# Kernel tuning notes

Measured on AMD Instinct MI355X. Metric: run time of the kernel, lower is better.

## Reference

```python
import jax, jax.numpy as jnp
import numpy as np

B, D, T = 32, 6, 2048
FH, ENC, H, CONF, NC, K = 128, 128, 256, 64, 10, 5


def setup_inputs() -> dict:
    key = jax.random.key(0)
    ks = iter(jax.random.split(key, 40))
    n = lambda shape, s=0.05: jax.random.normal(next(ks), shape, dtype=jnp.float32) * s
    inp = {
        'M': jax.random.normal(next(ks), (B, D, T), dtype=jnp.float32),
        # causal conv frontend (4 dilated convs, kernel 5)
        'conv_w0': n((FH, D, K)), 'conv_b0': n((FH,)),
        'conv_w1': n((FH, FH, K)), 'conv_b1': n((FH,)),
        'conv_w2': n((FH, FH, K)), 'conv_b2': n((FH,)),
        'conv_w3': n((FH, FH, K)), 'conv_b3': n((FH,)),
        # encoder projection
        'enc_w': n((ENC, FH)), 'enc_b': n((ENC,)),
        # selective state space
        'A': n((H, H), 0.01), 'ip_w': n((H, ENC)), 'ip_b': n((H,)),
        'state_bias': jnp.zeros((H,), jnp.float32),
        'op_w': n((H, H)), 'op_b': n((H,)),
        # classifier head
        'cls_w1': n((256, H)), 'cls_b1': n((256,)),
        'cls_w2': n((NC, 256)), 'cls_b2': n((NC,)),
        # metanet: 2*D -> 64 -> 128 -> confound_dim
        'mn_w1': n((64, 2 * D)), 'mn_b1': n((64,)),
        'mn_w2': n((128, 64)), 'mn_b2': n((128,)),
        'mn_w3': n((CONF, 128)), 'mn_b3': n((CONF,)),
        # frontdoor: confound_dim -> 128 -> ssm_hidden
        'fd_w1': n((128, CONF)), 'fd_b1': n((128,)),
        'fd_w2': n((H, 128)), 'fd_b2': n((H,)),
    }
    return inp


def _causal_conv(x, w, b, d):
    # x: (B,C,T), w: (O,I,K). pad-left (K-1)*d == pad-both + trim-right in torch code
    y = jax.lax.conv_general_dilated(
        x, w, window_strides=(1,), padding=[((w.shape[2] - 1) * d, 0)],
        rhs_dilation=(d,), dimension_numbers=('NCH', 'OIH', 'NCH'))
    return jax.nn.relu(y + b[None, :, None])


def reference(M, conv_w0, conv_b0, conv_w1, conv_b1, conv_w2, conv_b2, conv_w3, conv_b3,
              enc_w, enc_b, A, ip_w, ip_b, state_bias, op_w, op_b,
              cls_w1, cls_b1, cls_w2, cls_b2,
              mn_w1, mn_b1, mn_w2, mn_b2, mn_w3, mn_b3,
              fd_w1, fd_b1, fd_w2, fd_b2):
    # frontend: 4 causal dilated convs with ReLU
    out = M
    for w, b, d in ((conv_w0, conv_b0, 1), (conv_w1, conv_b1, 2),
                    (conv_w2, conv_b2, 4), (conv_w3, conv_b3, 8)):
        out = _causal_conv(out, w, b, d)
    feat = jnp.einsum('bct,ec->bte', out, enc_w) + enc_b  # (B,T,ENC)
    # SSM: precompute input projection, then sequential scan over T
    u = jnp.einsum('bte,he->bth', feat, ip_w) + ip_b + state_bias  # (B,T,H)

    def step(h, ut):
        h = jax.nn.gelu(h @ A.T + ut, approximate=False)
        return h, h

    h0 = jnp.zeros((M.shape[0], A.shape[0]), M.dtype)
    _, hs = jax.lax.scan(step, h0, jnp.swapaxes(u, 0, 1))  # hs: (T,B,H)
    ssm_out = jnp.einsum('tbh,gh->btg', hs, op_w) + op_b  # (B,T,H)
    pooled = ssm_out.mean(axis=1)  # (B,H)
    logits = jax.nn.relu(pooled @ cls_w1.T + cls_b1) @ cls_w2.T + cls_b2
    # confounder summary: mean & unbiased std over time
    s = jnp.concatenate([M.mean(axis=2), jnp.std(M, axis=2, ddof=1)], axis=1)
    z = jax.nn.relu(s @ mn_w1.T + mn_b1)
    z = jax.nn.relu(z @ mn_w2.T + mn_b2)
    conf_hat = z @ mn_w3.T + mn_b3
    adj = jax.nn.relu(conf_hat @ fd_w1.T + fd_b1) @ fd_w2.T + fd_b2
    corrected = pooled - adj
    return (logits, pooled, corrected, conf_hat)
```

## Files before the change

### kernel.cpp

```cpp
#include <hip/hip_runtime.h>
#include <cmath>


typedef __bf16 bf16_t;
typedef bf16_t bf16x8 __attribute__((ext_vector_type(8)));
typedef float f32x4 __attribute__((ext_vector_type(4)));

__device__ __forceinline__ f32x4 mfma16(bf16x8 a, bf16x8 b, f32x4 c) {
  return __builtin_amdgcn_mfma_f32_16x16x32_bf16(a, b, c, 0, 0, 0);
}

__device__ __forceinline__ float gelu_f(float x) {
  float a = x * 0.70710678118654752440f;
  float z = fabsf(a);
  float t = __builtin_amdgcn_rcpf(1.0f + 0.3275911f * z);
  float p = t * (0.254829592f +
            t * (-0.284496736f +
            t * (1.421413741f +
            t * (-1.453152027f +
            t * 1.061405429f))));
  float e = __expf(-z * z);
  float erf_a = __builtin_copysignf(1.0f - p * e, a);
  return 0.5f * x * (1.0f + erf_a);
}

__global__ void k_prep(const float* __restrict__ w0, const float* __restrict__ w1,
                       const float* __restrict__ w2, const float* __restrict__ w3,
                       const float* __restrict__ ip_w, const float* __restrict__ enc_w,
                       const float* __restrict__ enc_b, const float* __restrict__ ip_b,
                       const float* __restrict__ sbias,
                       bf16_t* __restrict__ wb0, bf16_t* __restrict__ wb1,
                       bf16_t* __restrict__ wb2, bf16_t* __restrict__ wb3,
                       bf16_t* __restrict__ wce, float* __restrict__ bce) {
  int bid = blockIdx.x;
  if (bid >= 976) {
    int idx = (bid - 976) * 256 + threadIdx.x;
    int h = idx >> 7, c = idx & 127;
    float s = 0.f;
    for (int e = 0; e < 128; ++e) s += ip_w[h * 128 + e] * enc_w[e * 128 + c];
    wce[h * 128 + c] = (bf16_t)s;
    if (c == 0) {
      float bv = 0.f;
      for (int e = 0; e < 128; ++e) bv += ip_w[h * 128 + e] * enc_b[e];
      bce[h] = bv + ip_b[h] + sbias[h];
    }
    return;
  }
  int idx = bid * 256 + threadIdx.x;
  if (idx < 128 * 32) {
    int o = idx >> 5, k = idx & 31;
    float v = 0.f;
    if (k < 30) { int i = k / 5, kk = k - i * 5; v = w0[(o * 6 + i) * 5 + kk]; }
    wb0[idx] = (bf16_t)v;
    return;
  }
  int e = idx - 128 * 32;
  if (e < 3 * 5 * 128 * 128) {
    int layer = e / (5 * 128 * 128);
    int r = e - layer * (5 * 128 * 128);
    int ks = r / 16384;
    int o = (r >> 7) & 127;
    int i = r & 127;
    const float* w = layer == 0 ? w1 : layer == 1 ? w2 : w3;
    bf16_t* wb = layer == 0 ? wb1 : layer == 1 ? wb2 : wb3;
    wb[r] = (bf16_t)w[(o * 128 + i) * 5 + ks];
  }
}

__global__ __launch_bounds__(256) void k_conv0(const float* __restrict__ M,
                                               const bf16_t* __restrict__ wb0,
                                               const float* __restrict__ b0,
                                               bf16_t* __restrict__ out) {
  __shared__ float raw[6][136];
  __shared__ bf16_t Xe[128 * 40];
  const int tid = threadIdx.x;
  const int b = blockIdx.y, t0 = blockIdx.x * 128;
  for (int id = tid; id < 6 * 132; id += 256) {
    int i = id / 132, j = id - i * 132;
    int t = t0 - 4 + j;
    raw[i][j] = (t >= 0) ? M[((size_t)b * 6 + i) * 2048 + t] : 0.f;
  }
  __syncthreads();
  for (int id = tid; id < 128 * 32; id += 256) {
    int tl = id >> 5, k = id & 31;
    float v = 0.f;
    if (k < 30) { int i = k / 5, kk = k - i * 5; v = raw[i][tl + kk]; }
    Xe[tl * 40 + k] = (bf16_t)v;
  }
  __syncthreads();
  const int w = tid >> 6, lane = tid & 63, q = lane >> 4, l15 = lane & 15;
  const int k0 = q * 8;
  const f32x4 z4 = {0.f, 0.f, 0.f, 0.f};
  f32x4 acc[2][8];
#pragma unroll
  for (int mt = 0; mt < 2; ++mt)
#pragma unroll
    for (int nt = 0; nt < 8; ++nt) acc[mt][nt] = z4;
  bf16x8 af[2];
#pragma unroll
  for (int mt = 0; mt < 2; ++mt)
    af[mt] = *(const bf16x8*)&Xe[(w * 32 + mt * 16 + l15) * 40 + k0];
#pragma unroll
  for (int nt = 0; nt < 8; ++nt) {
    bf16x8 bf = *(const bf16x8*)&wb0[(nt * 16 + l15) * 32 + k0];
#pragma unroll
    for (int mt = 0; mt < 2; ++mt) acc[mt][nt] = mfma16(af[mt], bf, acc[mt][nt]);
  }
#pragma unroll
  for (int nt = 0; nt < 8; ++nt) {
    const int o = nt * 16 + l15;
    const float bias = b0[o];
#pragma unroll
    for (int mt = 0; mt < 2; ++mt) {
#pragma unroll
      for (int r = 0; r < 4; ++r) {
        int t = t0 + w * 32 + mt * 16 + q * 4 + r;
        float v = acc[mt][nt][r] + bias;
        out[((size_t)b * 2048 + t) * 128 + o] = (bf16_t)(v > 0.f ? v : 0.f);
      }
    }
  }
}

template <int DIL>
__global__ __launch_bounds__(256) void k_conv(const bf16_t* __restrict__ in,
                                              const bf16_t* __restrict__ wb,
                                              const float* __restrict__ bias,
                                              bf16_t* __restrict__ out) {
  __shared__ bf16_t Xs[160 * 136];
  const int tid = threadIdx.x;
  const int b = blockIdx.y, t0 = blockIdx.x * 128;
  const bf16_t* src = in + (size_t)b * 2048 * 128;
  for (int id = tid; id < 160 * 16; id += 256) {
    int r = id >> 4, ck = id & 15;
    int t = t0 + r - 32;
    int4 v = make_int4(0, 0, 0, 0);
    if (t >= 0) v = *(const int4*)(src + (size_t)t * 128 + ck * 8);
    *(int4*)&Xs[r * 136 + ck * 8] = v;
  }
  __syncthreads();
  const int w = tid >> 6, lane = tid & 63, q = lane >> 4, l15 = lane & 15;
  const f32x4 z4 = {0.f, 0.f, 0.f, 0.f};
  f32x4 acc[2][8];
#pragma unroll
  for (int mt = 0; mt < 2; ++mt)
#pragma unroll
    for (int nt = 0; nt < 8; ++nt) acc[mt][nt] = z4;
#pragma unroll
  for (int ks = 0; ks < 5; ++ks) {
    const int shift = (4 - ks) * DIL;
#pragma unroll
    for (int kt = 0; kt < 4; ++kt) {
      const int k0 = kt * 32 + q * 8;
      bf16x8 af[2];
#pragma unroll
      for (int mt = 0; mt < 2; ++mt)
        af[mt] = *(const bf16x8*)&Xs[(32 + w * 32 + mt * 16 + l15 - shift) * 136 + k0];
#pragma unroll
      for (int nt = 0; nt < 8; ++nt) {
        bf16x8 bf = *(const bf16x8*)&wb[((size_t)ks * 128 + nt * 16 + l15) * 128 + k0];
#pragma unroll
        for (int mt = 0; mt < 2; ++mt) acc[mt][nt] = mfma16(af[mt], bf, acc[mt][nt]);
      }
    }
  }
#pragma unroll
  for (int nt = 0; nt < 8; ++nt) {
    const int o = nt * 16 + l15;
    const float bv = bias[o];
#pragma unroll
    for (int mt = 0; mt < 2; ++mt) {
#pragma unroll
      for (int r = 0; r < 4; ++r) {
        int t = t0 + w * 32 + mt * 16 + q * 4 + r;
        float v = acc[mt][nt][r] + bv;
        out[((size_t)b * 2048 + t) * 128 + o] = (bf16_t)(v > 0.f ? v : 0.f);
      }
    }
  }
}

__global__ __launch_bounds__(256) void k_ugemm(const bf16_t* __restrict__ in,
                                               const bf16_t* __restrict__ wce,
                                               const float* __restrict__ bce,
                                               bf16_t* __restrict__ u) {
  __shared__ bf16_t Xs[128 * 136];
  const int tid = threadIdx.x;
  const int b = blockIdx.y, t0 = blockIdx.x * 128, hh = blockIdx.z;
  const bf16_t* src = in + (size_t)b * 2048 * 128;
  for (int id = tid; id < 128 * 16; id += 256) {
    int r = id >> 4, ck = id & 15;
    *(int4*)&Xs[r * 136 + ck * 8] = *(const int4*)(src + (size_t)(t0 + r) * 128 + ck * 8);
  }
  __syncthreads();
  const int w = tid >> 6, lane = tid & 63, q = lane >> 4, l15 = lane & 15;
  const f32x4 z4 = {0.f, 0.f, 0.f, 0.f};
  f32x4 acc[2][8];
#pragma unroll
  for (int mt = 0; mt < 2; ++mt)
#pragma unroll
    for (int nt = 0; nt < 8; ++nt) acc[mt][nt] = z4;
#pragma unroll
  for (int kt = 0; kt < 4; ++kt) {
    const int k0 = kt * 32 + q * 8;
    bf16x8 af[2];
#pragma unroll
    for (int mt = 0; mt < 2; ++mt)
      af[mt] = *(const bf16x8*)&Xs[(w * 32 + mt * 16 + l15) * 136 + k0];
#pragma unroll
    for (int nt = 0; nt < 8; ++nt) {
      bf16x8 bf = *(const bf16x8*)&wce[((size_t)hh * 128 + nt * 16 + l15) * 128 + k0];
#pragma unroll
      for (int mt = 0; mt < 2; ++mt) acc[mt][nt] = mfma16(af[mt], bf, acc[mt][nt]);
    }
  }
#pragma unroll
  for (int nt = 0; nt < 8; ++nt) {
    const int h = hh * 128 + nt * 16 + l15;
    const float bv = bce[h];
#pragma unroll
    for (int mt = 0; mt < 2; ++mt) {
#pragma unroll
      for (int r = 0; r < 4; ++r) {
        int t = t0 + w * 32 + mt * 16 + q * 4 + r;
        u[((size_t)b * 2048 + t) * 256 + h] = (bf16_t)(acc[mt][nt][r] + bv);
      }
    }
  }
}

__global__ __launch_bounds__(256, 1) void k_scan(const float* __restrict__ Am,
                                                 const bf16_t* __restrict__ u,
                                                 float* __restrict__ hbarOut) {
  __shared__ bf16_t hb[2][256];
  const int b = blockIdx.x;
  const int tid = threadIdx.x;
  const int w = tid >> 6, lane = tid & 63, q = lane >> 4, l15 = lane & 15;

  bf16x8 bfr[4][8];
#pragma unroll
  for (int nt = 0; nt < 4; ++nt) {
    const int c = w * 64 + nt * 16 + l15;
#pragma unroll
    for (int kt = 0; kt < 8; ++kt) {
      const float* ap = Am + (size_t)c * 256 + kt * 32 + q * 8;
      f32x4 p0 = *(const f32x4*)ap;
      f32x4 p1 = *(const f32x4*)(ap + 4);
      bf16x8 v;
      v[0] = (bf16_t)p0[0]; v[1] = (bf16_t)p0[1]; v[2] = (bf16_t)p0[2]; v[3] = (bf16_t)p0[3];
      v[4] = (bf16_t)p1[0]; v[5] = (bf16_t)p1[1]; v[6] = (bf16_t)p1[2]; v[7] = (bf16_t)p1[3];
      bfr[nt][kt] = v;
    }
  }
  hb[0][tid] = (bf16_t)0.f;
  hb[1][tid] = (bf16_t)0.f;
  const bf16_t* up = u + (size_t)b * 2048 * 256 + tid;
  float hbar = 0.f;
  bf16_t ua = up[0];
  bf16_t ub = up[256];
  __syncthreads();

  const f32x4 z4 = {0.f, 0.f, 0.f, 0.f};

#define SCAN_STEP(RD, WR, UREG)                                   \
  {                                                               \
    bf16x8 af[8];                                                 \
    _Pragma("unroll")                                             \
    for (int kt = 0; kt < 8; ++kt)                                \
      af[kt] = *(const bf16x8*)&hb[RD][kt * 32 + q * 8];          \
    float uin = (float)(UREG);                                    \
    f32x4 acc[4];                                                 \
    _Pragma("unroll")                                             \
    for (int nt = 0; nt < 4; ++nt) {                              \
      acc[nt] = z4;                                               \
      acc[nt][0] = (q == nt) ? uin : 0.f;                         \
    }                                                             \
    _Pragma("unroll")                                             \
    for (int kt = 0; kt < 8; ++kt) {                              \
      _Pragma("unroll")                                           \
      for (int nt = 0; nt < 4; ++nt)                              \
        acc[nt] = mfma16(af[kt], bfr[nt][kt], acc[nt]);           \
    }                                                             \
    __builtin_amdgcn_sched_group_barrier(0x100, 8, 0);            \
    __builtin_amdgcn_sched_group_barrier(0x008, 32, 0);           \
    float y = (q == 0) ? acc[0][0] : (q == 1) ? acc[1][0]         \
            : (q == 2) ? acc[2][0] : acc[3][0];                   \
    float g = gelu_f(y);                                          \
    hb[WR][tid] = (bf16_t)g;                                      \
    asm volatile("s_waitcnt lgkmcnt(0)" ::: "memory");            \
    __builtin_amdgcn_s_barrier();                                 \
    __builtin_amdgcn_sched_barrier(0);                            \
    hbar += g;                                                    \
  }

  for (int t = 0; t < 2048; t += 2) {
    bf16_t ua2 = (t + 2 < 2048) ? up[(size_t)(t + 2) * 256] : (bf16_t)0.f;
    SCAN_STEP(0, 1, ua)
    bf16_t ub2 = (t + 3 < 2048) ? up[(size_t)(t + 3) * 256] : (bf16_t)0.f;
    SCAN_STEP(1, 0, ub)
    ua = ua2;
    ub = ub2;
  }
#undef SCAN_STEP

  hbarOut[b * 256 + tid] = hbar * (1.f / 2048.f);
}

__global__ __launch_bounds__(256) void k_post(
    const float* __restrict__ M, const float* __restrict__ hbar,
    const float* __restrict__ w1, const float* __restrict__ b1,
    const float* __restrict__ w2, const float* __restrict__ b2,
    const float* __restrict__ w3, const float* __restrict__ b3,
    const float* __restrict__ f1, const float* __restrict__ fb1,
    const float* __restrict__ f2, const float* __restrict__ fb2,
    const float* __restrict__ op_w, const float* __restrict__ op_b,
    const float* __restrict__ cw1, const float* __restrict__ cb1,
    const float* __restrict__ cw2, const float* __restrict__ cb2,
    float* __restrict__ out) {
  const int b = blockIdx.x, tid = threadIdx.x;
  const int w = tid >> 6, lane = tid & 63;
  __shared__ float s12[12], z1[64], z2[128], ch[64], a1[128], adjs[256];
  __shared__ float hs[256], ps[256], hid[256];
  __shared__ float as_[4], ass_[4];
  for (int c = 0; c < 6; ++c) {
    const float* p = M + ((size_t)b * 6 + c) * 2048;
    float s = 0.f, ss = 0.f;
    for (int t = tid; t < 2048; t += 256) { float v = p[t]; s += v; ss += v * v; }
    for (int o = 32; o > 0; o >>= 1) { s += __shfl_down(s, o, 64); ss += __shfl_down(ss, o, 64); }
    if (lane == 0) { as_[w] = s; ass_[w] = ss; }
    __syncthreads();
    if (tid == 0) {
      s = as_[0] + as_[1] + as_[2] + as_[3];
      ss = ass_[0] + ass_[1] + ass_[2] + ass_[3];
      float mean = s * (1.f / 2048.f);
      float var = (ss - 2048.f * mean * mean) * (1.f / 2047.f);
      if (var < 0.f) var = 0.f;
      s12[c] = mean;
      s12[6 + c] = sqrtf(var);
    }
    __syncthreads();
  }
  if (tid < 64) {
    float v = b1[tid];
    for (int e = 0; e < 12; ++e) v += w1[tid * 12 + e] * s12[e];
    z1[tid] = v > 0.f ? v : 0.f;
  }
  __syncthreads();
  if (tid < 128) {
    float v = b2[tid];
    for (int e = 0; e < 64; ++e) v += w2[tid * 64 + e] * z1[e];
    z2[tid] = v > 0.f ? v : 0.f;
  }
  __syncthreads();
  if (tid < 64) {
    float v = b3[tid];
    for (int e = 0; e < 128; ++e) v += w3[tid * 128 + e] * z2[e];
    ch[tid] = v;
    out[16704 + b * 64 + tid] = v;
  }
  __syncthreads();
  if (tid < 128) {
    float v = fb1[tid];
    for (int e = 0; e < 64; ++e) v += f1[tid * 64 + e] * ch[e];
    a1[tid] = v > 0.f ? v : 0.f;
  }
  __syncthreads();
  {
    float v = fb2[tid];
    for (int e = 0; e < 128; ++e) v += f2[tid * 128 + e] * a1[e];
    adjs[tid] = v;
  }
  hs[tid] = hbar[b * 256 + tid];
  __syncthreads();
  float v = op_b[tid];
  for (int h = 0; h < 256; ++h) v += op_w[tid * 256 + h] * hs[h];
  out[320 + b * 256 + tid] = v;
  out[8512 + b * 256 + tid] = v - adjs[tid];
  ps[tid] = v;
  __syncthreads();
  float hv = cb1[tid];
  for (int h = 0; h < 256; ++h) hv += cw1[tid * 256 + h] * ps[h];
  hid[tid] = hv > 0.f ? hv : 0.f;
  __syncthreads();
  if (tid < 10) {
    float lv = cb2[tid];
    for (int h = 0; h < 256; ++h) lv += cw2[tid * 256 + h] * hid[h];
    out[b * 10 + tid] = lv;
  }
}

extern "C" void kernel_launch(void* const* d_in, const int* in_sizes, int n_in,
                              void* d_out, int out_size, void* d_ws, size_t ws_size,
                              hipStream_t stream) {
  (void)in_sizes; (void)n_in; (void)out_size; (void)ws_size;
  const float* M    = (const float*)d_in[0];
  const float* w0   = (const float*)d_in[1];  const float* b0  = (const float*)d_in[2];
  const float* w1   = (const float*)d_in[3];  const float* b1  = (const float*)d_in[4];
  const float* w2   = (const float*)d_in[5];  const float* b2  = (const float*)d_in[6];
  const float* w3   = (const float*)d_in[7];  const float* b3  = (const float*)d_in[8];
  const float* encw = (const float*)d_in[9];  const float* encb = (const float*)d_in[10];
  const float* Am   = (const float*)d_in[11];
  const float* ipw  = (const float*)d_in[12]; const float* ipb = (const float*)d_in[13];
  const float* sb   = (const float*)d_in[14];
  const float* opw  = (const float*)d_in[15]; const float* opb = (const float*)d_in[16];
  const float* cw1  = (const float*)d_in[17]; const float* cb1 = (const float*)d_in[18];
  const float* cw2  = (const float*)d_in[19]; const float* cb2 = (const float*)d_in[20];
  const float* mw1  = (const float*)d_in[21]; const float* mb1 = (const float*)d_in[22];
  const float* mw2  = (const float*)d_in[23]; const float* mb2 = (const float*)d_in[24];
  const float* mw3  = (const float*)d_in[25]; const float* mb3 = (const float*)d_in[26];
  const float* fw1  = (const float*)d_in[27]; const float* fb1 = (const float*)d_in[28];
  const float* fw2  = (const float*)d_in[29]; const float* fb2 = (const float*)d_in[30];
  float* out = (float*)d_out;

  char* ws = (char*)d_ws;
  bf16_t* wb0  = (bf16_t*)(ws + 0);
  bf16_t* wb1  = (bf16_t*)(ws + 8192);
  bf16_t* wb2  = (bf16_t*)(ws + 172032);
  bf16_t* wb3  = (bf16_t*)(ws + 335872);
  bf16_t* wce  = (bf16_t*)(ws + 499712);
  float*  bce  = (float*) (ws + 565248);
  float*  hbar = (float*) (ws + 566272);
  bf16_t* actA = (bf16_t*)(ws + 633856);
  bf16_t* actB = (bf16_t*)(ws + 17411072);
  bf16_t* u    = (bf16_t*)(ws + 34188288);

  k_prep<<<1104, 256, 0, stream>>>(w0, w1, w2, w3, ipw, encw, encb, ipb, sb,
                                   wb0, wb1, wb2, wb3, wce, bce);
  k_conv0<<<dim3(16, 32), 256, 0, stream>>>(M, wb0, b0, actA);
  k_conv<2><<<dim3(16, 32), 256, 0, stream>>>(actA, wb1, b1, actB);
  k_conv<4><<<dim3(16, 32), 256, 0, stream>>>(actB, wb2, b2, actA);
  k_conv<8><<<dim3(16, 32), 256, 0, stream>>>(actA, wb3, b3, actB);
  k_ugemm<<<dim3(16, 32, 2), 256, 0, stream>>>(actB, wce, bce, u);
  k_scan<<<32, 256, 0, stream>>>(Am, u, hbar);
  k_post<<<32, 256, 0, stream>>>(M, hbar, mw1, mb1, mw2, mb2, mw3, mb3,
                                 fw1, fb1, fw2, fb2, opw, opb,
                                 cw1, cb1, cw2, cb2, out);
}
```

Baseline: 1.407 ms.

## Split scan step across 16 waves with one output tile per wave

The sequential SSM scan block grows from 4 to 16 waves. Each wave now owns a single 16-column tile of A and issues 8 MFMAs per step instead of 32, so the per-step dependent chain is shorter and the matrix work is spread over more SIMDs. In exchange the per-step block barrier now synchronises 16 waves instead of 4, and only a quarter of the lanes do useful GELU and stores.

```diff
diff --git a/kernel.cpp b/kernel.cpp
--- a/kernel.cpp
+++ b/kernel.cpp
@@ -229,32 +229,31 @@
   }
 }
 
-__global__ __launch_bounds__(256, 1) void k_scan(const float* __restrict__ Am,
-                                                 const bf16_t* __restrict__ u,
-                                                 float* __restrict__ hbarOut) {
+__global__ __launch_bounds__(1024, 1) void k_scan(const float* __restrict__ Am,
+                                                  const bf16_t* __restrict__ u,
+                                                  float* __restrict__ hbarOut) {
   __shared__ bf16_t hb[2][256];
   const int b = blockIdx.x;
   const int tid = threadIdx.x;
   const int w = tid >> 6, lane = tid & 63, q = lane >> 4, l15 = lane & 15;
-
-  bf16x8 bfr[4][8];
-#pragma unroll
-  for (int nt = 0; nt < 4; ++nt) {
-    const int c = w * 64 + nt * 16 + l15;
-#pragma unroll
-    for (int kt = 0; kt < 8; ++kt) {
-      const float* ap = Am + (size_t)c * 256 + kt * 32 + q * 8;
-      f32x4 p0 = *(const f32x4*)ap;
-      f32x4 p1 = *(const f32x4*)(ap + 4);
-      bf16x8 v;
-      v[0] = (bf16_t)p0[0]; v[1] = (bf16_t)p0[1]; v[2] = (bf16_t)p0[2]; v[3] = (bf16_t)p0[3];
-      v[4] = (bf16_t)p1[0]; v[5] = (bf16_t)p1[1]; v[6] = (bf16_t)p1[2]; v[7] = (bf16_t)p1[3];
-      bfr[nt][kt] = v;
-    }
-  }
-  hb[0][tid] = (bf16_t)0.f;
-  hb[1][tid] = (bf16_t)0.f;
-  const bf16_t* up = u + (size_t)b * 2048 * 256 + tid;
+  const int c = w * 16 + l15;
+
+  bf16x8 bfr[8];
+#pragma unroll
+  for (int kt = 0; kt < 8; ++kt) {
+    const float* ap = Am + (size_t)c * 256 + kt * 32 + q * 8;
+    f32x4 p0 = *(const f32x4*)ap;
+    f32x4 p1 = *(const f32x4*)(ap + 4);
+    bf16x8 v;
+    v[0] = (bf16_t)p0[0]; v[1] = (bf16_t)p0[1]; v[2] = (bf16_t)p0[2]; v[3] = (bf16_t)p0[3];
+    v[4] = (bf16_t)p1[0]; v[5] = (bf16_t)p1[1]; v[6] = (bf16_t)p1[2]; v[7] = (bf16_t)p1[3];
+    bfr[kt] = v;
+  }
+  if (tid < 256) {
+    hb[0][tid] = (bf16_t)0.f;
+    hb[1][tid] = (bf16_t)0.f;
+  }
+  const bf16_t* up = u + (size_t)b * 2048 * 256 + c;
   float hbar = 0.f;
   bf16_t ua = up[0];
   bf16_t ub = up[256];
@@ -269,24 +268,15 @@
     for (int kt = 0; kt < 8; ++kt)                                \
       af[kt] = *(const bf16x8*)&hb[RD][kt * 32 + q * 8];          \
     float uin = (float)(UREG);                                    \
-    f32x4 acc[4];                                                 \
+    f32x4 acc = z4;                                               \
+    acc[0] = uin;                                                 \
     _Pragma("unroll")                                             \
-    for (int nt = 0; nt < 4; ++nt) {                              \
-      acc[nt] = z4;                                               \
-      acc[nt][0] = (q == nt) ? uin : 0.f;                         \
-    }                                                             \
-    _Pragma("unroll")                                             \
-    for (int kt = 0; kt < 8; ++kt) {                              \
-      _Pragma("unroll")                                           \
-      for (int nt = 0; nt < 4; ++nt)                              \
-        acc[nt] = mfma16(af[kt], bfr[nt][kt], acc[nt]);           \
-    }                                                             \
+    for (int kt = 0; kt < 8; ++kt)                                \
+      acc = mfma16(af[kt], bfr[kt], acc);                         \
     __builtin_amdgcn_sched_group_barrier(0x100, 8, 0);            \
-    __builtin_amdgcn_sched_group_barrier(0x008, 32, 0);           \
-    float y = (q == 0) ? acc[0][0] : (q == 1) ? acc[1][0]         \
-            : (q == 2) ? acc[2][0] : acc[3][0];                   \
-    float g = gelu_f(y);                                          \
-    hb[WR][tid] = (bf16_t)g;                                      \
+    __builtin_amdgcn_sched_group_barrier(0x008, 8, 0);            \
+    float g = gelu_f(acc[0]);                                     \
+    if (q == 0) hb[WR][c] = (bf16_t)g;                            \
     asm volatile("s_waitcnt lgkmcnt(0)" ::: "memory");            \
     __builtin_amdgcn_s_barrier();                                 \
     __builtin_amdgcn_sched_barrier(0);                            \
@@ -303,7 +293,7 @@
   }
 #undef SCAN_STEP
 
-  hbarOut[b * 256 + tid] = hbar * (1.f / 2048.f);
+  if (q == 0) hbarOut[b * 256 + c] = hbar * (1.f / 2048.f);
 }
 
 __global__ __launch_bounds__(256) void k_post(
@@ -431,7 +421,7 @@
   k_conv<4><<<dim3(16, 32), 256, 0, stream>>>(actB, wb2, b2, actA);
   k_conv<8><<<dim3(16, 32), 256, 0, stream>>>(actA, wb3, b3, actB);
   k_ugemm<<<dim3(16, 32, 2), 256, 0, stream>>>(actB, wce, bce, u);
-  k_scan<<<32, 256, 0, stream>>>(Am, u, hbar);
+  k_scan<<<32, 1024, 0, stream>>>(Am, u, hbar);
   k_post<<<32, 256, 0, stream>>>(M, hbar, mw1, mb1, mw2, mb2, mw3, mb3,
                                  fw1, fb1, fw2, fb2, opw, opb,
                                  cw1, cb1, cw2, cb2, out);
```

Result: slower. 1.465 ms (+4.2%).

## Process two batch sequences per scan block to interleave independent recurrences

Applied to the files above, without the earlier changes.

The sequential scan kernel now handles two batch elements per workgroup, launching 16 blocks instead of 32. Each step issues MFMAs for both independent recurrences, so one chain's latency can hide behind the other's and the per-step barrier cost is shared. The price is half as many active CUs, twice the MFMA work per block per step, and the explicit sched_group_barrier hints are removed.

```diff
diff --git a/kernel.cpp b/kernel.cpp
--- a/kernel.cpp
+++ b/kernel.cpp
@@ -232,8 +232,8 @@
 __global__ __launch_bounds__(256, 1) void k_scan(const float* __restrict__ Am,
                                                  const bf16_t* __restrict__ u,
                                                  float* __restrict__ hbarOut) {
-  __shared__ bf16_t hb[2][256];
-  const int b = blockIdx.x;
+  __shared__ bf16_t hb[2][2][256];
+  const int b0 = blockIdx.x * 2, b1 = b0 + 1;
   const int tid = threadIdx.x;
   const int w = tid >> 6, lane = tid & 63, q = lane >> 4, l15 = lane & 15;
 
@@ -252,58 +252,68 @@
       bfr[nt][kt] = v;
     }
   }
-  hb[0][tid] = (bf16_t)0.f;
-  hb[1][tid] = (bf16_t)0.f;
-  const bf16_t* up = u + (size_t)b * 2048 * 256 + tid;
-  float hbar = 0.f;
-  bf16_t ua = up[0];
-  bf16_t ub = up[256];
+  hb[0][0][tid] = (bf16_t)0.f;
+  hb[0][1][tid] = (bf16_t)0.f;
+  hb[1][0][tid] = (bf16_t)0.f;
+  hb[1][1][tid] = (bf16_t)0.f;
+  const bf16_t* up0 = u + (size_t)b0 * 2048 * 256 + tid;
+  const bf16_t* up1 = u + (size_t)b1 * 2048 * 256 + tid;
+  float hbar0 = 0.f, hbar1 = 0.f;
+  bf16_t ua0 = up0[0], ub0 = up0[256];
+  bf16_t ua1 = up1[0], ub1 = up1[256];
   __syncthreads();
 
   const f32x4 z4 = {0.f, 0.f, 0.f, 0.f};
 
-#define SCAN_STEP(RD, WR, UREG)                                   \
+#define SCAN_STEP(RD, WR, U0, U1)                                 \
   {                                                               \
-    bf16x8 af[8];                                                 \
-    _Pragma("unroll")                                             \
-    for (int kt = 0; kt < 8; ++kt)                                \
-      af[kt] = *(const bf16x8*)&hb[RD][kt * 32 + q * 8];          \
-    float uin = (float)(UREG);                                    \
-    f32x4 acc[4];                                                 \
+    float uin0 = (float)(U0), uin1 = (float)(U1);                 \
+    f32x4 acc0[4], acc1[4];                                       \
     _Pragma("unroll")                                             \
     for (int nt = 0; nt < 4; ++nt) {                              \
-      acc[nt] = z4;                                               \
-      acc[nt][0] = (q == nt) ? uin : 0.f;                         \
+      acc0[nt] = z4; acc0[nt][0] = (q == nt) ? uin0 : 0.f;        \
+      acc1[nt] = z4; acc1[nt][0] = (q == nt) ? uin1 : 0.f;        \
     }                                                             \
     _Pragma("unroll")                                             \
     for (int kt = 0; kt < 8; ++kt) {                              \
+      bf16x8 af0 = *(const bf16x8*)&hb[RD][0][kt * 32 + q * 8];   \
+      bf16x8 af1 = *(const bf16x8*)&hb[RD][1][kt * 32 + q * 8];   \
       _Pragma("unroll")                                           \
       for (int nt = 0; nt < 4; ++nt)                              \
-        acc[nt] = mfma16(af[kt], bfr[nt][kt], acc[nt]);           \
+        acc0[nt] = mfma16(af0, bfr[nt][kt], acc0[nt]);            \
+      _Pragma("unroll")                                           \
+      for (int nt = 0; nt < 4; ++nt)                              \
+        acc1[nt] = mfma16(af1, bfr[nt][kt], acc1[nt]);            \
     }                                                             \
-    __builtin_amdgcn_sched_group_barrier(0x100, 8, 0);            \
-    __builtin_amdgcn_sched_group_barrier(0x008, 32, 0);           \
-    float y = (q == 0) ? acc[0][0] : (q == 1) ? acc[1][0]         \
-            : (q == 2) ? acc[2][0] : acc[3][0];                   \
-    float g = gelu_f(y);                                          \
-    hb[WR][tid] = (bf16_t)g;                                      \
+    float y0 = (q == 0) ? acc0[0][0] : (q == 1) ? acc0[1][0]      \
+             : (q == 2) ? acc0[2][0] : acc0[3][0];                \
+    float y1 = (q == 0) ? acc1[0][0] : (q == 1) ? acc1[1][0]      \
+             : (q == 2) ? acc1[2][0] : acc1[3][0];                \
+    float g0 = gelu_f(y0);                                        \
+    float g1 = gelu_f(y1);                                        \
+    hb[WR][0][tid] = (bf16_t)g0;                                  \
+    hb[WR][1][tid] = (bf16_t)g1;                                  \
     asm volatile("s_waitcnt lgkmcnt(0)" ::: "memory");            \
     __builtin_amdgcn_s_barrier();                                 \
     __builtin_amdgcn_sched_barrier(0);                            \
-    hbar += g;                                                    \
+    hbar0 += g0;                                                  \
+    hbar1 += g1;                                                  \
   }
 
   for (int t = 0; t < 2048; t += 2) {
-    bf16_t ua2 = (t + 2 < 2048) ? up[(size_t)(t + 2) * 256] : (bf16_t)0.f;
-    SCAN_STEP(0, 1, ua)
-    bf16_t ub2 = (t + 3 < 2048) ? up[(size_t)(t + 3) * 256] : (bf16_t)0.f;
-    SCAN_STEP(1, 0, ub)
-    ua = ua2;
-    ub = ub2;
+    bf16_t ua0n = (t + 2 < 2048) ? up0[(size_t)(t + 2) * 256] : (bf16_t)0.f;
+    bf16_t ua1n = (t + 2 < 2048) ? up1[(size_t)(t + 2) * 256] : (bf16_t)0.f;
+    SCAN_STEP(0, 1, ua0, ua1)
+    bf16_t ub0n = (t + 3 < 2048) ? up0[(size_t)(t + 3) * 256] : (bf16_t)0.f;
+    bf16_t ub1n = (t + 3 < 2048) ? up1[(size_t)(t + 3) * 256] : (bf16_t)0.f;
+    SCAN_STEP(1, 0, ub0, ub1)
+    ua0 = ua0n; ua1 = ua1n;
+    ub0 = ub0n; ub1 = ub1n;
   }
 #undef SCAN_STEP
 
-  hbarOut[b * 256 + tid] = hbar * (1.f / 2048.f);
+  hbarOut[b0 * 256 + tid] = hbar0 * (1.f / 2048.f);
+  hbarOut[b1 * 256 + tid] = hbar1 * (1.f / 2048.f);
 }
 
 __global__ __launch_bounds__(256) void k_post(
@@ -431,7 +441,7 @@
   k_conv<4><<<dim3(16, 32), 256, 0, stream>>>(actB, wb2, b2, actA);
   k_conv<8><<<dim3(16, 32), 256, 0, stream>>>(actA, wb3, b3, actB);
   k_ugemm<<<dim3(16, 32, 2), 256, 0, stream>>>(actB, wce, bce, u);
-  k_scan<<<32, 256, 0, stream>>>(Am, u, hbar);
+  k_scan<<<16, 256, 0, stream>>>(Am, u, hbar);
   k_post<<<32, 256, 0, stream>>>(M, hbar, mw1, mb1, mw2, mb2, mw3, mb3,
                                  fw1, fb1, fw2, fb2, opw, opb,
                                  cw1, cb1, cw2, cb2, out);
```

Result: slower. 2.443 ms (+73.7%).
